# Optimization experiments

Measured on AMD Instinct MI355X. Metric: run time of the kernel, lower is better.

The kernel has to match this reference:

```python
import jax, jax.numpy as jnp
import numpy as np

B, S, H, L = 32, 2048, 768, 9


def setup_inputs() -> dict:
    key = jax.random.key(0)
    k0, k1, k2, k3, k4, k5 = jax.random.split(key, 6)
    return {
        "hidden_states": jax.random.normal(k0, (B, S, H), jnp.float32),
        "W": jax.random.normal(k1, (L, H), jnp.float32) * 0.02,
        "b": jnp.zeros((L,), jnp.float32),
        "start_transitions": jax.random.uniform(k2, (L,), jnp.float32, -0.1, 0.1),
        "end_transitions": jax.random.uniform(k3, (L,), jnp.float32, -0.1, 0.1),
        "transitions": jax.random.uniform(k4, (L, L), jnp.float32, -0.1, 0.1),
        "labels": jax.random.randint(k5, (B, S), 0, L).astype(jnp.int64),
        "attention_mask": jnp.ones((B, S), jnp.int32),
    }


def _crf_neg_log_likelihood(emissions, tags, mask, start_transitions, end_transitions, transitions):
    # emissions: [B,S,L], tags: [B,S] int, mask: [B,S] bool (mask[:,0] assumed True)
    Bsz = emissions.shape[0]
    em_t = jnp.swapaxes(emissions, 0, 1)          # [S,B,L]
    tags_t = jnp.swapaxes(tags, 0, 1)             # [S,B]
    mask_t = jnp.swapaxes(mask, 0, 1).astype(emissions.dtype)  # [S,B]
    barange = jnp.arange(Bsz)

    # ---- numerator: score of the gold path (pytorch-crf _compute_score) ----
    score0 = start_transitions[tags_t[0]] + em_t[0][barange, tags_t[0]]  # [B]

    def num_step(score, x):
        em_i, tag_prev, tag_i, m_i = x
        step = transitions[tag_prev, tag_i] + em_i[barange, tag_i]
        return score + step * m_i, None

    score, _ = jax.lax.scan(num_step, score0,
                            (em_t[1:], tags_t[:-1], tags_t[1:], mask_t[1:]))
    seq_ends = jnp.sum(mask, axis=1).astype(jnp.int32) - 1              # [B]
    last_tags = jnp.take_along_axis(tags, seq_ends[:, None], axis=1)[:, 0]
    score = score + end_transitions[last_tags]

    # ---- denominator: log partition (forward algorithm) ----
    alpha0 = start_transitions[None, :] + em_t[0]  # [B,L]

    def den_step(alpha, x):
        em_i, m_i = x
        # alpha[b,i] + transitions[i,j] + em_i[b,j] -> logsumexp over i
        nxt = jax.nn.logsumexp(alpha[:, :, None] + transitions[None, :, :]
                               + em_i[:, None, :], axis=1)
        alpha = jnp.where(m_i[:, None] > 0, nxt, alpha)
        return alpha, None

    alpha, _ = jax.lax.scan(den_step, alpha0, (em_t[1:], mask_t[1:]))
    denom = jax.nn.logsumexp(alpha + end_transitions[None, :], axis=1)  # [B]

    llh = score - denom
    return -jnp.mean(llh)  # reduction='mean', loss = -log_likelihood


def reference(hidden_states, W, b, start_transitions, end_transitions, transitions, labels, attention_mask):
    # classifier over backbone hidden states
    emissions = jnp.einsum('bsh,lh->bsl', hidden_states, W) + b  # [B,S,L]
    label_mask = labels != -100
    lab = jnp.where(labels == -100, 0, labels)
    loss = _crf_neg_log_likelihood(emissions, lab, label_mask,
                                   start_transitions, end_transitions, transitions)
    return loss, emissions
```

## Files before the change

kernel.cpp:

```cpp
#include <hip/hip_runtime.h>

#define BB 32
#define SS 2048
#define HH 768
#define LL 9
#define NROWS (BB * SS)
#define NCHUNK 64
#define TCHUNK 32
#define RPB 8
#define PASSES 4
#define GEMM_BLOCKS (NROWS / RPB)

__device__ __forceinline__ float lse9(const float* v) {
  float m = fmaxf(fmaxf(fmaxf(fmaxf(v[0], v[1]), fmaxf(v[2], v[3])),
                        fmaxf(fmaxf(v[4], v[5]), fmaxf(v[6], v[7]))),
                  v[8]);
  float s = 0.f;
#pragma unroll
  for (int k = 0; k < 9; ++k) s += __expf(v[k] - m);
  return m + __logf(s);
}

__global__ __launch_bounds__(256, 4)
void emis_gemm(const float* __restrict__ hs, const float* __restrict__ W,
               const float* __restrict__ bias, float* __restrict__ em,
               int* __restrict__ gcnt) {
  const int tid = threadIdx.x;
  const int lane = tid & 63;
  const int w = tid >> 6;
  const int pair = w >> 1;
  const int half = w & 1;
  const int rowbase = blockIdx.x * RPB;
  const int kb = half * 384;
  if (blockIdx.x == 0 && tid == 0) *gcnt = 0;

  __shared__ float part[RPB][129][9];

  float wr[LL][6];
#pragma unroll
  for (int l = 0; l < LL; ++l) {
    float4 t4 = *reinterpret_cast<const float4*>(W + l * HH + kb + lane * 4);
    float2 t2 = *reinterpret_cast<const float2*>(W + l * HH + kb + 256 + lane * 2);
    wr[l][0] = t4.x; wr[l][1] = t4.y; wr[l][2] = t4.z; wr[l][3] = t4.w;
    wr[l][4] = t2.x; wr[l][5] = t2.y;
  }

  const int Lp = half * 64 + lane;
  const float* rA = hs + (size_t)(rowbase + 0 + pair) * HH + kb;
  float4 A4 = *reinterpret_cast<const float4*>(rA + lane * 4);
  float2 A2 = *reinterpret_cast<const float2*>(rA + 256 + lane * 2);
  const float* rB = hs + (size_t)(rowbase + 2 + pair) * HH + kb;
  float4 B4 = *reinterpret_cast<const float4*>(rB + lane * 4);
  float2 B2 = *reinterpret_cast<const float2*>(rB + 256 + lane * 2);

#pragma unroll
  for (int p = 0; p < PASSES; ++p) {
    float4 cur4 = (p & 1) ? B4 : A4;
    float2 cur2 = (p & 1) ? B2 : A2;
    if (p + 2 < PASSES) {
      const float* rn = hs + (size_t)(rowbase + (p + 2) * 2 + pair) * HH + kb;
      if (p & 1) {
        B4 = *reinterpret_cast<const float4*>(rn + lane * 4);
        B2 = *reinterpret_cast<const float2*>(rn + 256 + lane * 2);
      } else {
        A4 = *reinterpret_cast<const float4*>(rn + lane * 4);
        A2 = *reinterpret_cast<const float2*>(rn + 256 + lane * 2);
      }
    }
    const float h[6] = {cur4.x, cur4.y, cur4.z, cur4.w, cur2.x, cur2.y};
    const int o = p * 2 + pair;
#pragma unroll
    for (int l = 0; l < LL; ++l) {
      float s = h[0] * wr[l][0];
#pragma unroll
      for (int q = 1; q < 6; ++q) s = fmaf(h[q], wr[l][q], s);
      part[o][Lp][l] = s;
    }
  }
  __syncthreads();

  if (tid < RPB * LL) {
    const int o = tid / LL, l = tid - o * LL;
    float s = bias[l];
#pragma unroll 8
    for (int q = 0; q < 128; ++q) s += part[o][q][l];
    em[(size_t)(rowbase + o) * LL + l] = s;
  }
}

__global__ __launch_bounds__(128)
void crf_chunk(const float* __restrict__ em, const int* __restrict__ lab,
               const float* __restrict__ trans, const float* __restrict__ startT,
               float* __restrict__ Pout, float* __restrict__ numpart,
               int* __restrict__ cntpart) {
  const int blk = blockIdx.x;
  const int b = blk >> 6, c = blk & 63;
  const int tid = threadIdx.x;
  const int lane = tid & 63;
  const int wv = tid >> 6;
  __shared__ float em_s[TCHUNK * LL];
  __shared__ int lab_s[TCHUNK + 1];
  __shared__ float Pbuf[2][81];

  const int t0 = c * TCHUNK;
  const size_t ebase = (size_t)(b * SS + t0) * LL;
  for (int i = tid; i < TCHUNK * LL; i += 128) em_s[i] = em[ebase + i];
  if (tid <= TCHUNK) {
    int g = t0 - 1 + tid;
    lab_s[tid] = (g >= 0) ? lab[b * SS + g] : 0;
  }
  const int i9 = tid / 9, j9 = tid % 9;
  float tc[9];
  if (tid < 81) {
#pragma unroll
    for (int k = 0; k < 9; ++k) tc[k] = trans[k * 9 + j9];
  }
  __syncthreads();

  unsigned long long mb =
      __ballot((lane < 32) ? (lab_s[1 + lane] != -100) : false);
  unsigned mask32 = (unsigned)mb;

  if (wv == 1) {
    float sc = 0.f;
    if (lane < 32) {
      int lv = lab_s[1 + lane];
      int tg = (lv != -100) ? lv : 0;
      if (t0 + lane == 0) {
        sc = startT[tg] + em_s[tg];
      } else if (lv != -100) {
        int pv = lab_s[lane];
        int tp = (pv != -100) ? pv : 0;
        sc = trans[tp * LL + tg] + em_s[lane * LL + tg];
      }
    }
#pragma unroll
    for (int off = 32; off; off >>= 1) sc += __shfl_xor(sc, off, 64);
    if (lane == 0) {
      numpart[blk] = sc;
      cntpart[blk] = __popc(mask32);
    }
  }

  if (tid < 81) Pbuf[0][tid] = (i9 == j9) ? 0.f : -1e30f;
  __syncthreads();
  int cur = 0;
  const int ltstart = (c == 0) ? 1 : 0;
  for (int lt = ltstart; lt < TCHUNK; ++lt) {
    if ((mask32 >> lt) & 1u) {
      if (tid < 81) {
        float v[9];
#pragma unroll
        for (int k = 0; k < 9; ++k) v[k] = Pbuf[cur][i9 * 9 + k] + tc[k];
        Pbuf[cur ^ 1][tid] = lse9(v) + em_s[lt * LL + j9];
      }
      __syncthreads();
      cur ^= 1;
    }
  }
  if (tid < 81) Pout[(size_t)blk * 81 + tid] = Pbuf[cur][tid];
}

__global__ __launch_bounds__(128)
void crf_fold(const float* __restrict__ Pm, const float* __restrict__ em,
              const float* __restrict__ startT, const float* __restrict__ endT,
              const float* __restrict__ numpart, const int* __restrict__ cntpart,
              const int* __restrict__ lab, float* __restrict__ llh,
              int* __restrict__ gcnt, float* __restrict__ out) {
  const int b = blockIdx.x, tid = threadIdx.x;
  __shared__ __align__(16) float Abuf[64 * 81];
  __shared__ __align__(16) float Bbuf[32 * 81];

  const float* src = Pm + (size_t)b * NCHUNK * 81;
  for (int i = tid; i < 64 * 81 / 4; i += 128)
    reinterpret_cast<float4*>(Abuf)[i] = reinterpret_cast<const float4*>(src)[i];
  __syncthreads();

  float* pin = Abuf;
  float* pout = Bbuf;
  for (int n = 32;; n >>= 1) {
    for (int o = tid; o < n * 81; o += 128) {
      int m = o / 81, e = o % 81;
      int i = e / 9, j = e % 9;
      const float* M1 = pin + (2 * m) * 81;
      const float* M2 = pin + (2 * m + 1) * 81;
      float v[9];
#pragma unroll
      for (int k = 0; k < 9; ++k) v[k] = M1[i * 9 + k] + M2[k * 9 + j];
      pout[o] = lse9(v);
    }
    __syncthreads();
    if (n == 1) break;
    float* t = pin; pin = pout;
    pout = (pout == Bbuf) ? Abuf : t;
  }
  const float* fin = pout;

  float ns = 0.f;
  int cn = 0;
  if (tid < 64) {
    ns = numpart[b * 64 + tid];
    cn = cntpart[b * 64 + tid];
#pragma unroll
    for (int off = 32; off; off >>= 1) {
      ns += __shfl_xor(ns, off, 64);
      cn += __shfl_xor(cn, off, 64);
    }
  }
  if (tid == 0) {
    float a0[9], af[9], v[9];
#pragma unroll
    for (int j = 0; j < 9; ++j) a0[j] = startT[j] + em[(size_t)b * SS * LL + j];
#pragma unroll
    for (int j = 0; j < 9; ++j) {
#pragma unroll
      for (int k = 0; k < 9; ++k) v[k] = a0[k] + fin[k * 9 + j];
      af[j] = lse9(v);
    }
#pragma unroll
    for (int j = 0; j < 9; ++j) v[j] = af[j] + endT[j];
    float den = lse9(v);
    int se = cn - 1;
    int lt = lab[b * SS + se];
    if (lt == -100) lt = 0;
    llh[b] = (ns + endT[lt]) - den;

    __threadfence();
    int old = atomicAdd(gcnt, 1);
    if (old == BB - 1) {
      __threadfence();
      float s = 0.f;
      for (int i = 0; i < BB; ++i)
        s += __hip_atomic_load(&llh[i], __ATOMIC_RELAXED,
                               __HIP_MEMORY_SCOPE_AGENT);
      out[0] = -s / (float)BB;
    }
  }
}

extern "C" void kernel_launch(void* const* d_in, const int* in_sizes, int n_in,
                              void* d_out, int out_size, void* d_ws, size_t ws_size,
                              hipStream_t stream) {
  const float* hs = (const float*)d_in[0];
  const float* W = (const float*)d_in[1];
  const float* bias = (const float*)d_in[2];
  const float* startT = (const float*)d_in[3];
  const float* endT = (const float*)d_in[4];
  const float* trans = (const float*)d_in[5];
  const int* labels = (const int*)d_in[6];

  float* out = (float*)d_out;
  float* em = out + 1;

  float* wsf = (float*)d_ws;
  float* llh = wsf;
  int* gcnt = (int*)(wsf + 32);
  float* numpart = wsf + 64;
  int* cntpart = (int*)(wsf + 64 + 2048);
  float* Pm = wsf + 64 + 4096;

  emis_gemm<<<GEMM_BLOCKS, 256, 0, stream>>>(hs, W, bias, em, gcnt);
  crf_chunk<<<BB * NCHUNK, 128, 0, stream>>>(em, labels, trans, startT,
                                             Pm, numpart, cntpart);
  crf_fold<<<BB, 128, 0, stream>>>(Pm, em, startT, endT, numpart, cntpart,
                                   labels, llh, gcnt, out);
}
```

Measured before the change: 82.51 us.

## Fuse emission GEMM with per-chunk CRF scan and reduce partials via DPP

Merges the emission projection kernel and the chunked CRF transfer-matrix kernel into one kernel, where each block computes emissions for its 32 time steps and then runs the chunk scan from shared memory. Partial dot products are reduced with DPP cross-lane adds over 16 lanes instead of a 129-entry shared-memory reduction. This removes one launch and the global round-trip of emissions between the kernels. In exchange, the grid shrinks to 2048 blocks of 256 threads, and the serial 32-step scan now runs inside the bandwidth-bound GEMM block, which may hurt overlap and occupancy.

```diff
diff --git a/kernel.cpp b/kernel.cpp
--- a/kernel.cpp
+++ b/kernel.cpp
@@ -7,9 +7,6 @@
 #define NROWS (BB * SS)
 #define NCHUNK 64
 #define TCHUNK 32
-#define RPB 8
-#define PASSES 4
-#define GEMM_BLOCKS (NROWS / RPB)
 
 __device__ __forceinline__ float lse9(const float* v) {
   float m = fmaxf(fmaxf(fmaxf(fmaxf(v[0], v[1]), fmaxf(v[2], v[3])),
@@ -21,21 +18,47 @@
   return m + __logf(s);
 }
 
+template <int CTRL>
+__device__ __forceinline__ float dpp_add(float x) {
+  int t = __builtin_amdgcn_update_dpp(0, __float_as_int(x), CTRL, 0xf, 0xf, true);
+  return x + __int_as_float(t);
+}
+__device__ __forceinline__ float red16(float x) {
+  x = dpp_add<0xB1>(x);
+  x = dpp_add<0x4E>(x);
+  x = dpp_add<0x141>(x);
+  x = dpp_add<0x140>(x);
+  return x;
+}
+
 __global__ __launch_bounds__(256, 4)
-void emis_gemm(const float* __restrict__ hs, const float* __restrict__ W,
-               const float* __restrict__ bias, float* __restrict__ em,
-               int* __restrict__ gcnt) {
+void emcrf(const float* __restrict__ hs, const float* __restrict__ W,
+           const float* __restrict__ bias, const int* __restrict__ lab,
+           const float* __restrict__ trans, const float* __restrict__ startT,
+           float* __restrict__ em, float* __restrict__ Pout,
+           float* __restrict__ numpart, int* __restrict__ cntpart,
+           int* __restrict__ gcnt) {
+  const int blk = blockIdx.x;
+  const int b = blk >> 6, c = blk & 63;
   const int tid = threadIdx.x;
   const int lane = tid & 63;
   const int w = tid >> 6;
-  const int pair = w >> 1;
   const int half = w & 1;
-  const int rowbase = blockIdx.x * RPB;
+  const int rowg = (w >> 1) * 16;
+  const int t0 = c * TCHUNK;
+  if (blk == 0 && tid == 0) *gcnt = 0;
+
+  __shared__ float part[TCHUNK][8][9];
+  __shared__ float em_s[TCHUNK * LL];
+  __shared__ float Pbuf[2][81];
+  __shared__ int lab_s[TCHUNK + 1];
+
+  if (tid <= TCHUNK) {
+    int g = t0 - 1 + tid;
+    lab_s[tid] = (g >= 0) ? lab[b * SS + g] : 0;
+  }
+
   const int kb = half * 384;
-  if (blockIdx.x == 0 && tid == 0) *gcnt = 0;
-
-  __shared__ float part[RPB][129][9];
-
   float wr[LL][6];
 #pragma unroll
   for (int l = 0; l < LL; ++l) {
@@ -45,21 +68,24 @@
     wr[l][4] = t2.x; wr[l][5] = t2.y;
   }
 
-  const int Lp = half * 64 + lane;
-  const float* rA = hs + (size_t)(rowbase + 0 + pair) * HH + kb;
-  float4 A4 = *reinterpret_cast<const float4*>(rA + lane * 4);
-  float2 A2 = *reinterpret_cast<const float2*>(rA + 256 + lane * 2);
-  const float* rB = hs + (size_t)(rowbase + 2 + pair) * HH + kb;
-  float4 B4 = *reinterpret_cast<const float4*>(rB + lane * 4);
-  float2 B2 = *reinterpret_cast<const float2*>(rB + 256 + lane * 2);
-
-#pragma unroll
-  for (int p = 0; p < PASSES; ++p) {
-    float4 cur4 = (p & 1) ? B4 : A4;
-    float2 cur2 = (p & 1) ? B2 : A2;
-    if (p + 2 < PASSES) {
-      const float* rn = hs + (size_t)(rowbase + (p + 2) * 2 + pair) * HH + kb;
-      if (p & 1) {
+  const size_t rbase = (size_t)(b * SS + t0 + rowg) * HH + kb;
+  const float* r0 = hs + rbase;
+  float4 A4 = *reinterpret_cast<const float4*>(r0 + lane * 4);
+  float2 A2 = *reinterpret_cast<const float2*>(r0 + 256 + lane * 2);
+  const float* r1 = hs + rbase + HH;
+  float4 B4 = *reinterpret_cast<const float4*>(r1 + lane * 4);
+  float2 B2 = *reinterpret_cast<const float2*>(r1 + 256 + lane * 2);
+
+  const int slot = half * 4 + (lane >> 4);
+  const bool wlead = (lane & 15) == 0;
+
+#pragma unroll
+  for (int r = 0; r < 16; ++r) {
+    float4 cur4 = (r & 1) ? B4 : A4;
+    float2 cur2 = (r & 1) ? B2 : A2;
+    if (r + 2 < 16) {
+      const float* rn = hs + rbase + (size_t)(r + 2) * HH;
+      if (r & 1) {
         B4 = *reinterpret_cast<const float4*>(rn + lane * 4);
         B2 = *reinterpret_cast<const float2*>(rn + 256 + lane * 2);
       } else {
@@ -68,60 +94,32 @@
       }
     }
     const float h[6] = {cur4.x, cur4.y, cur4.z, cur4.w, cur2.x, cur2.y};
-    const int o = p * 2 + pair;
 #pragma unroll
     for (int l = 0; l < LL; ++l) {
       float s = h[0] * wr[l][0];
 #pragma unroll
       for (int q = 1; q < 6; ++q) s = fmaf(h[q], wr[l][q], s);
-      part[o][Lp][l] = s;
-    }
-  }
-  __syncthreads();
-
-  if (tid < RPB * LL) {
-    const int o = tid / LL, l = tid - o * LL;
+      s = red16(s);
+      if (wlead) part[rowg + r][slot][l] = s;
+    }
+  }
+  __syncthreads();
+
+  float* emg = em + (size_t)(b * SS + t0) * LL;
+  for (int j = tid; j < TCHUNK * LL; j += 256) {
+    const int o = j / LL, l = j - o * LL;
     float s = bias[l];
-#pragma unroll 8
-    for (int q = 0; q < 128; ++q) s += part[o][q][l];
-    em[(size_t)(rowbase + o) * LL + l] = s;
-  }
-}
-
-__global__ __launch_bounds__(128)
-void crf_chunk(const float* __restrict__ em, const int* __restrict__ lab,
-               const float* __restrict__ trans, const float* __restrict__ startT,
-               float* __restrict__ Pout, float* __restrict__ numpart,
-               int* __restrict__ cntpart) {
-  const int blk = blockIdx.x;
-  const int b = blk >> 6, c = blk & 63;
-  const int tid = threadIdx.x;
-  const int lane = tid & 63;
-  const int wv = tid >> 6;
-  __shared__ float em_s[TCHUNK * LL];
-  __shared__ int lab_s[TCHUNK + 1];
-  __shared__ float Pbuf[2][81];
-
-  const int t0 = c * TCHUNK;
-  const size_t ebase = (size_t)(b * SS + t0) * LL;
-  for (int i = tid; i < TCHUNK * LL; i += 128) em_s[i] = em[ebase + i];
-  if (tid <= TCHUNK) {
-    int g = t0 - 1 + tid;
-    lab_s[tid] = (g >= 0) ? lab[b * SS + g] : 0;
-  }
-  const int i9 = tid / 9, j9 = tid % 9;
-  float tc[9];
-  if (tid < 81) {
-#pragma unroll
-    for (int k = 0; k < 9; ++k) tc[k] = trans[k * 9 + j9];
-  }
-  __syncthreads();
-
-  unsigned long long mb =
-      __ballot((lane < 32) ? (lab_s[1 + lane] != -100) : false);
-  unsigned mask32 = (unsigned)mb;
-
-  if (wv == 1) {
+#pragma unroll
+    for (int q = 0; q < 8; ++q) s += part[o][q][l];
+    em_s[j] = s;
+    emg[j] = s;
+  }
+  __syncthreads();
+
+  unsigned mask32 =
+      (unsigned)__ballot((lane < 32) ? (lab_s[1 + lane] != -100) : false);
+
+  if (w == 2) {
     float sc = 0.f;
     if (lane < 32) {
       int lv = lab_s[1 + lane];
@@ -142,7 +140,13 @@
     }
   }
 
-  if (tid < 81) Pbuf[0][tid] = (i9 == j9) ? 0.f : -1e30f;
+  const int i9 = tid / 9, j9 = tid % 9;
+  float tc[9];
+  if (tid < 81) {
+#pragma unroll
+    for (int k = 0; k < 9; ++k) tc[k] = trans[k * 9 + j9];
+    Pbuf[0][tid] = (i9 == j9) ? 0.f : -1e30f;
+  }
   __syncthreads();
   int cur = 0;
   const int ltstart = (c == 0) ? 1 : 0;
@@ -259,9 +263,8 @@
   int* cntpart = (int*)(wsf + 64 + 2048);
   float* Pm = wsf + 64 + 4096;
 
-  emis_gemm<<<GEMM_BLOCKS, 256, 0, stream>>>(hs, W, bias, em, gcnt);
-  crf_chunk<<<BB * NCHUNK, 128, 0, stream>>>(em, labels, trans, startT,
-                                             Pm, numpart, cntpart);
+  emcrf<<<BB * NCHUNK, 256, 0, stream>>>(hs, W, bias, labels, trans, startT,
+                                         em, Pm, numpart, cntpart, gcnt);
   crf_fold<<<BB, 128, 0, stream>>>(Pm, em, startT, endT, numpart, cntpart,
                                    labels, llh, gcnt, out);
 }
```

Result: faster. 79.91 us (-3.1%).

## Compute emissions GEMM with split-bf16 MFMA instead of scalar FMAs

Applied to the files above, without the earlier changes.

Replaces the scalar-FMA emission projection with a matrix-core kernel that uses 16x16x32 bf16 MFMAs. Each wave handles 16 rows, and W is pre-split into hi/lo bf16 parts in shared memory. Three MFMAs per step (hi*hi, lo*hi, hi*lo) approximate fp32 accuracy. The aim is to cut ALU issue cost in a memory-bound GEMM, at the price of per-block W conversion overhead and padded 16-column tiles of which only 9 are used.

```diff
diff --git a/kernel.cpp b/kernel.cpp
--- a/kernel.cpp
+++ b/kernel.cpp
@@ -7,9 +7,11 @@
 #define NROWS (BB * SS)
 #define NCHUNK 64
 #define TCHUNK 32
-#define RPB 8
-#define PASSES 4
-#define GEMM_BLOCKS (NROWS / RPB)
+#define NSTEP 24
+#define ZSLOT (NSTEP * 36)
+
+typedef short s16x8 __attribute__((ext_vector_type(8)));
+typedef float f32x4 __attribute__((ext_vector_type(4)));
 
 __device__ __forceinline__ float lse9(const float* v) {
   float m = fmaxf(fmaxf(fmaxf(fmaxf(v[0], v[1]), fmaxf(v[2], v[3])),
@@ -21,70 +23,99 @@
   return m + __logf(s);
 }
 
-__global__ __launch_bounds__(256, 4)
-void emis_gemm(const float* __restrict__ hs, const float* __restrict__ W,
+__device__ __forceinline__ unsigned cvtpk(float a, float b) {
+  unsigned d;
+  asm("v_cvt_pk_bf16_f32 %0, %1, %2" : "=v"(d) : "v"(a), "v"(b));
+  return d;
+}
+
+__device__ __forceinline__ void split8(const float* f, unsigned* hi,
+                                       unsigned* lo) {
+#pragma unroll
+  for (int p = 0; p < 4; ++p) {
+    unsigned h = cvtpk(f[2 * p], f[2 * p + 1]);
+    float h0 = __uint_as_float(h << 16);
+    float h1 = __uint_as_float(h & 0xffff0000u);
+    lo[p] = cvtpk(f[2 * p] - h0, f[2 * p + 1] - h1);
+    hi[p] = h;
+  }
+}
+
+__global__ __launch_bounds__(256, 3)
+void emis_mfma(const float* __restrict__ hs, const float* __restrict__ W,
                const float* __restrict__ bias, float* __restrict__ em,
                int* __restrict__ gcnt) {
   const int tid = threadIdx.x;
+  if (blockIdx.x == 0 && tid == 0) *gcnt = 0;
+
+  __shared__ uint4 Bhi[ZSLOT + 1];
+  __shared__ uint4 Blo[ZSLOT + 1];
+
+  for (int s = tid; s <= ZSLOT; s += 256) {
+    float f[8] = {0.f, 0.f, 0.f, 0.f, 0.f, 0.f, 0.f, 0.f};
+    if (s < ZSLOT) {
+      const int kk = s / 36, rem = s - kk * 36;
+      const int kg = rem / 9, col = rem - kg * 9;
+      const float* wp = W + col * HH + kk * 32 + kg * 8;
+      float4 w0 = *reinterpret_cast<const float4*>(wp);
+      float4 w1 = *reinterpret_cast<const float4*>(wp + 4);
+      f[0] = w0.x; f[1] = w0.y; f[2] = w0.z; f[3] = w0.w;
+      f[4] = w1.x; f[5] = w1.y; f[6] = w1.z; f[7] = w1.w;
+    }
+    unsigned hi[4], lo[4];
+    split8(f, hi, lo);
+    Bhi[s] = make_uint4(hi[0], hi[1], hi[2], hi[3]);
+    Blo[s] = make_uint4(lo[0], lo[1], lo[2], lo[3]);
+  }
+  __syncthreads();
+
   const int lane = tid & 63;
   const int w = tid >> 6;
-  const int pair = w >> 1;
-  const int half = w & 1;
-  const int rowbase = blockIdx.x * RPB;
-  const int kb = half * 384;
-  if (blockIdx.x == 0 && tid == 0) *gcnt = 0;
-
-  __shared__ float part[RPB][129][9];
-
-  float wr[LL][6];
-#pragma unroll
-  for (int l = 0; l < LL; ++l) {
-    float4 t4 = *reinterpret_cast<const float4*>(W + l * HH + kb + lane * 4);
-    float2 t2 = *reinterpret_cast<const float2*>(W + l * HH + kb + 256 + lane * 2);
-    wr[l][0] = t4.x; wr[l][1] = t4.y; wr[l][2] = t4.z; wr[l][3] = t4.w;
-    wr[l][4] = t2.x; wr[l][5] = t2.y;
-  }
-
-  const int Lp = half * 64 + lane;
-  const float* rA = hs + (size_t)(rowbase + 0 + pair) * HH + kb;
-  float4 A4 = *reinterpret_cast<const float4*>(rA + lane * 4);
-  float2 A2 = *reinterpret_cast<const float2*>(rA + 256 + lane * 2);
-  const float* rB = hs + (size_t)(rowbase + 2 + pair) * HH + kb;
-  float4 B4 = *reinterpret_cast<const float4*>(rB + lane * 4);
-  float2 B2 = *reinterpret_cast<const float2*>(rB + 256 + lane * 2);
-
-#pragma unroll
-  for (int p = 0; p < PASSES; ++p) {
-    float4 cur4 = (p & 1) ? B4 : A4;
-    float2 cur2 = (p & 1) ? B2 : A2;
-    if (p + 2 < PASSES) {
-      const float* rn = hs + (size_t)(rowbase + (p + 2) * 2 + pair) * HH + kb;
-      if (p & 1) {
-        B4 = *reinterpret_cast<const float4*>(rn + lane * 4);
-        B2 = *reinterpret_cast<const float2*>(rn + 256 + lane * 2);
-      } else {
-        A4 = *reinterpret_cast<const float4*>(rn + lane * 4);
-        A2 = *reinterpret_cast<const float2*>(rn + 256 + lane * 2);
-      }
-    }
-    const float h[6] = {cur4.x, cur4.y, cur4.z, cur4.w, cur2.x, cur2.y};
-    const int o = p * 2 + pair;
-#pragma unroll
-    for (int l = 0; l < LL; ++l) {
-      float s = h[0] * wr[l][0];
-#pragma unroll
-      for (int q = 1; q < 6; ++q) s = fmaf(h[q], wr[l][q], s);
-      part[o][Lp][l] = s;
-    }
-  }
-  __syncthreads();
-
-  if (tid < RPB * LL) {
-    const int o = tid / LL, l = tid - o * LL;
-    float s = bias[l];
-#pragma unroll 8
-    for (int q = 0; q < 128; ++q) s += part[o][q][l];
-    em[(size_t)(rowbase + o) * LL + l] = s;
+  const int l15 = lane & 15;
+  const int kg = lane >> 4;
+  const int tile = blockIdx.x * 4 + w;
+
+  const float* ab = hs + (size_t)(tile * 16 + l15) * HH + kg * 8;
+  const int s0 = (l15 < 9) ? (kg * 9 + l15) : ZSLOT;
+  const int sst = (l15 < 9) ? 36 : 0;
+  const float bv = (l15 < 9) ? bias[l15] : 0.f;
+
+  f32x4 acc = {0.f, 0.f, 0.f, 0.f};
+  float4 pf[3][2];
+#pragma unroll
+  for (int q = 0; q < 3; ++q) {
+    pf[q][0] = *reinterpret_cast<const float4*>(ab + q * 32);
+    pf[q][1] = *reinterpret_cast<const float4*>(ab + q * 32 + 4);
+  }
+
+#pragma unroll
+  for (int kk = 0; kk < NSTEP; ++kk) {
+    const float4 u0 = pf[kk % 3][0];
+    const float4 u1 = pf[kk % 3][1];
+    if (kk + 3 < NSTEP) {
+      pf[kk % 3][0] = *reinterpret_cast<const float4*>(ab + (kk + 3) * 32);
+      pf[kk % 3][1] = *reinterpret_cast<const float4*>(ab + (kk + 3) * 32 + 4);
+    }
+    float f[8] = {u0.x, u0.y, u0.z, u0.w, u1.x, u1.y, u1.z, u1.w};
+    unsigned ah[4], al[4];
+    split8(f, ah, al);
+    const uint4 bh4 = Bhi[s0 + kk * sst];
+    const uint4 bl4 = Blo[s0 + kk * sst];
+    const s16x8 Ah = __builtin_bit_cast(s16x8, make_uint4(ah[0], ah[1], ah[2], ah[3]));
+    const s16x8 Al = __builtin_bit_cast(s16x8, make_uint4(al[0], al[1], al[2], al[3]));
+    const s16x8 Bh = __builtin_bit_cast(s16x8, bh4);
+    const s16x8 Bl = __builtin_bit_cast(s16x8, bl4);
+    acc = __builtin_amdgcn_mfma_f32_16x16x32_bf16(Ah, Bh, acc, 0, 0, 0);
+    acc = __builtin_amdgcn_mfma_f32_16x16x32_bf16(Al, Bh, acc, 0, 0, 0);
+    acc = __builtin_amdgcn_mfma_f32_16x16x32_bf16(Ah, Bl, acc, 0, 0, 0);
+  }
+
+  if (l15 < 9) {
+    float* o = em + (size_t)(tile * 16 + kg * 4) * LL + l15;
+    o[0] = acc[0] + bv;
+    o[LL] = acc[1] + bv;
+    o[2 * LL] = acc[2] + bv;
+    o[3 * LL] = acc[3] + bv;
   }
 }
 
@@ -117,9 +148,8 @@
   }
   __syncthreads();
 
-  unsigned long long mb =
-      __ballot((lane < 32) ? (lab_s[1 + lane] != -100) : false);
-  unsigned mask32 = (unsigned)mb;
+  unsigned mask32 =
+      (unsigned)__ballot((lane < 32) ? (lab_s[1 + lane] != -100) : false);
 
   if (wv == 1) {
     float sc = 0.f;
@@ -259,7 +289,7 @@
   int* cntpart = (int*)(wsf + 64 + 2048);
   float* Pm = wsf + 64 + 4096;
 
-  emis_gemm<<<GEMM_BLOCKS, 256, 0, stream>>>(hs, W, bias, em, gcnt);
+  emis_mfma<<<NROWS / 64, 256, 0, stream>>>(hs, W, bias, em, gcnt);
   crf_chunk<<<BB * NCHUNK, 128, 0, stream>>>(em, labels, trans, startT,
                                              Pm, numpart, cntpart);
   crf_fold<<<BB, 128, 0, stream>>>(Pm, em, startT, endT, numpart, cntpart,
```

Measured after the change: 77.74 us. -5.8%, faster.
